# Kernel optimization log

Hardware: AMD Instinct MI355X
Metric: run time of the kernel (lower is better)

Reference implementation:

```python
import jax, jax.numpy as jnp
import numpy as np

T, R, I = 16384, 1024, 128   # time steps, reservoir size, input size
CONN, SR = 0.05, 0.9         # connectivity_rate, spectral_radius


def _make_reservoir(rng):
    # Faithful to ESN.create_reservoir_weights: uniform[0,1), sparsify by
    # connectivity_rate, rescale to target spectral radius, flip half the
    # entries' signs.
    W = rng.random((R, R)).astype(np.float32)
    W[rng.random((R, R)) > CONN] = 0.0
    cur_sr = np.max(np.abs(np.linalg.eigvals(W)))
    W = W * (SR / cur_sr)
    neg = rng.choice(R * R, (R * R) // 2, replace=False)
    Wf = W.reshape(-1).copy()
    Wf[neg] *= -1.0
    return Wf.reshape(R, R).astype(np.float32)


def setup_inputs() -> dict:
    rng = np.random.default_rng(0)
    W_res = jnp.asarray(_make_reservoir(rng))
    key = jax.random.key(0)
    k1, k2 = jax.random.split(key)
    X = jax.random.normal(k1, (T, I), dtype=jnp.float32)
    # nn.init.uniform_(w, a=-1, b=1)
    W_in = jax.random.uniform(k2, (R, I), dtype=jnp.float32, minval=-1.0, maxval=1.0)
    state0 = jnp.zeros((R,), dtype=jnp.float32)
    return {"X": X, "W_in": W_in, "W_res": W_res, "state0": state0}


def reference(X, W_in, W_res, state0):
    # state_t = tanh(W_in @ x_t + W_res @ state_{t-1}); collect all states (T, R).
    # Input projections are independent across time -> one big GEMM up front.
    U = X @ W_in.T  # (T, R)

    def step(s, u):
        s = jnp.tanh(u + W_res @ s)
        return s, s

    _, all_states = jax.lax.scan(step, state0, U)
    return all_states  # (T, R), matches update_state's all_states
```

## Files before the change

kernel.cpp:

```cpp
#include <hip/hip_runtime.h>
#include <hip/hip_bf16.h>
#include <stdint.h>


constexpr int T_N = 16384;
constexpr int R_N = 1024;
constexpr int I_N = 128;

constexpr int BT = 64, BR = 64;

__global__ __launch_bounds__(256) void gemm_u_kernel(
    const float* __restrict__ X, const float* __restrict__ Win,
    float* __restrict__ U)
{
    __shared__ float XS[BT][68];
    __shared__ float WS[BR][68];
    const int tid = threadIdx.x;
    const int ty = tid >> 4, tx = tid & 15;
    const int t0 = blockIdx.x * BT;
    const int r0 = blockIdx.y * BR;
    float acc[4][4] = {};

    for (int k0 = 0; k0 < I_N; k0 += 64) {
        for (int idx = tid; idx < BT * 16; idx += 256) {
            int row = idx >> 4, c4 = (idx & 15) << 2;
            *reinterpret_cast<float4*>(&XS[row][c4]) =
                *reinterpret_cast<const float4*>(&X[(size_t)(t0 + row) * I_N + k0 + c4]);
        }
        for (int idx = tid; idx < BR * 16; idx += 256) {
            int row = idx >> 4, c4 = (idx & 15) << 2;
            *reinterpret_cast<float4*>(&WS[row][c4]) =
                *reinterpret_cast<const float4*>(&Win[(size_t)(r0 + row) * I_N + k0 + c4]);
        }
        __syncthreads();
#pragma unroll
        for (int k = 0; k < 64; k += 4) {
            float4 a[4], b[4];
#pragma unroll
            for (int i = 0; i < 4; ++i)
                a[i] = *reinterpret_cast<const float4*>(&XS[ty + 16 * i][k]);
#pragma unroll
            for (int jj = 0; jj < 4; ++jj)
                b[jj] = *reinterpret_cast<const float4*>(&WS[tx + 16 * jj][k]);
#pragma unroll
            for (int i = 0; i < 4; ++i)
#pragma unroll
                for (int jj = 0; jj < 4; ++jj)
                    acc[i][jj] += a[i].x * b[jj].x + a[i].y * b[jj].y +
                                  a[i].z * b[jj].z + a[i].w * b[jj].w;
        }
        __syncthreads();
    }
#pragma unroll
    for (int i = 0; i < 4; ++i)
#pragma unroll
        for (int jj = 0; jj < 4; ++jj)
            U[(size_t)(t0 + ty + 16 * i) * R_N + (r0 + tx + 16 * jj)] = acc[i][jj];
}

constexpr int GBLK    = 8;
constexpr int NLAUNCH = 64;
constexpr int B2      = 1024;
constexpr int RPB     = R_N / GBLK;
constexpr int TPR     = 8;
constexpr int KMAX    = 96;
constexpr int NSL     = KMAX / TPR;
constexpr int PCAP    = 1 << 20;

__device__ __forceinline__ float fast_tanh(float x) {
    float ax = fabsf(x);
    float e  = __expf(-2.0f * ax);
    float y  = (1.0f - e) / (1.0f + e);
    return copysignf(y, x);
}

__device__ __forceinline__ uint32_t l2_atomic_read(uint32_t* addr) {
    uint32_t old;
    asm volatile("global_atomic_add %0, %1, %2, off sc0\n\t"
                 "s_waitcnt vmcnt(0)"
                 : "=v"(old) : "v"(addr), "v"(0u) : "memory");
    return old;
}

__device__ __forceinline__ void l2_store_u32(uint32_t* addr, uint32_t v) {
    asm volatile("global_store_dword %0, %1, off"
                 :: "v"(addr), "v"(v) : "memory");
}

__global__ __launch_bounds__(1024) void esn_scan_kernel(
    const float* __restrict__ Wres, const float* __restrict__ state0,
    float* out, uint32_t* hdr, uint32_t* slots)
{
    __shared__ int   s_role;
    __shared__ float sbufA[2][R_N];
    __shared__ float sbufB[2][R_N];
    __shared__ uint2 ell[RPB][KMAX];
    __shared__ int   cnt[RPB];
    __shared__ int   rowmap[RPB];
    __shared__ int   hist[KMAX + 1];

    const int tid = threadIdx.x;

    if (tid == 0) {
        uint32_t xcd;
        asm volatile("s_getreg_b32 %0, hwreg(HW_REG_XCC_ID)" : "=s"(xcd));
        xcd &= 7u;
        uint32_t rank = __hip_atomic_fetch_add(&hdr[xcd], 1u,
                            __ATOMIC_RELAXED, __HIP_MEMORY_SCOPE_AGENT);
        int role = -1;
        if (rank < (uint32_t)GBLK) {
            if (rank == (uint32_t)(GBLK - 1)) {
                uint32_t expected = 0u;
                __hip_atomic_compare_exchange_strong(&hdr[8], &expected, xcd + 1u,
                    __ATOMIC_RELAXED, __ATOMIC_RELAXED, __HIP_MEMORY_SCOPE_AGENT);
            }
            uint32_t win = 0; int sp = 0;
            do {
                win = __hip_atomic_load(&hdr[8], __ATOMIC_RELAXED,
                                        __HIP_MEMORY_SCOPE_AGENT);
            } while (win == 0u && ++sp < PCAP);
            if (win == xcd + 1u) role = (int)rank;
        }
        s_role = role;
    }
    __syncthreads();
    const int b = s_role;
    if (b < 0) return;
    const int row0 = b * RPB;

    if (tid < RPB) cnt[tid] = 0;
    __syncthreads();
    for (int idx = tid; idx < RPB * R_N; idx += B2) {
        int r = idx >> 10, c = idx & (R_N - 1);
        float w = Wres[(size_t)(row0 + r) * R_N + c];
        if (w != 0.0f) {
            int slot = atomicAdd(&cnt[r], 1);
            if (slot < KMAX) ell[r][slot] = make_uint2((uint32_t)c, __float_as_uint(w));
        }
    }
    __syncthreads();

    if (tid <= KMAX) hist[tid] = 0;
    __syncthreads();
    if (tid < RPB) atomicAdd(&hist[min(cnt[tid], KMAX)], 1);
    __syncthreads();
    if (tid == 0) {
        int run = 0;
        for (int i = 0; i <= KMAX; ++i) { int c = hist[i]; hist[i] = run; run += c; }
    }
    __syncthreads();
    if (tid < RPB) {
        int c = min(cnt[tid], KMAX);
        int pos = atomicAdd(&hist[c], 1);
        rowmap[pos] = tid;
    }
    __syncthreads();

    const int rloc = rowmap[tid >> 3];
    const int j    = tid & 7;
    const int row  = row0 + rloc;
    const bool oddlane = (tid & 1) != 0;
    int   cols[NSL];
    float vals[NSL];
    int   kw;
    {
        int myn = cnt[rloc];
        if (myn > KMAX) myn = KMAX;
        int kcnt = (myn > j) ? (((myn - 1 - j) >> 3) + 1) : 0;
#pragma unroll
        for (int k = 0; k < NSL; ++k) {
            int slot = j + k * TPR;
            if (slot < myn) {
                uint2 e = ell[rloc][slot];
                int c = (int)e.x;
                if (oddlane) c = (c + 1) & (R_N - 1);
                cols[k] = c;
                vals[k] = __uint_as_float(e.y);
            } else { cols[k] = 0; vals[k] = 0.0f; }
        }
        kw = kcnt;
#pragma unroll
        for (int off = 1; off < 64; off <<= 1) {
            int o = __shfl_xor(kw, off, 64);
            kw = (o > kw) ? o : kw;
        }
        kw = __builtin_amdgcn_readfirstlane(kw);
    }

    sbufA[1][tid] = state0[tid];
    sbufB[1][(tid + 1) & (R_N - 1)] = state0[tid];
    float u_cur = (j == 0) ? out[row] : 0.0f;
    __syncthreads();

    for (int t = 0; t < T_N; ++t) {
        const int p = (t - 1) & 1;

        float u_next = 0.0f;
        if (j == 0 && t + 1 < T_N) u_next = out[(size_t)(t + 1) * R_N + row];

        if (t > 0 && (tid >> 7) != b) {
            uint32_t* slot = slots + ((size_t)p << 10) + tid;
            const uint32_t want8 = (uint32_t)(t & 0xFF);
            uint32_t w; int sp = 0;
            do { w = l2_atomic_read(slot);
            } while ((w & 0xFFu) != want8 && ++sp < PCAP);
            float v = __uint_as_float(w & 0xFFFFFF00u);
            sbufA[p][tid] = v;
            sbufB[p][(tid + 1) & (R_N - 1)] = v;
        }
        __syncthreads();

        const float* sb = oddlane ? sbufB[p] : sbufA[p];
        float acc = 0.0f;
#pragma unroll
        for (int k = 0; k < NSL; ++k) {
            if (k >= kw) break;
            acc = fmaf(vals[k], sb[cols[k]], acc);
        }

        acc += __shfl_xor(acc, 1, TPR);
        acc += __shfl_xor(acc, 2, TPR);
        acc += __shfl_xor(acc, 4, TPR);

        if (j == 0) {
            float y = fast_tanh(u_cur + acc);
            uint32_t bits = __float_as_uint(y);
            uint32_t pkt  = ((bits + 0x80u) & 0xFFFFFF00u)
                          | ((uint32_t)(t + 1) & 0xFFu);
            l2_store_u32(slots + ((size_t)(t & 1) << 10) + row, pkt);
            out[(size_t)t * R_N + row] = y;
            sbufA[t & 1][row] = y;
            sbufB[t & 1][(row + 1) & (R_N - 1)] = y;
        }
        u_cur = u_next;
    }
}

extern "C" void kernel_launch(void* const* d_in, const int* in_sizes, int n_in,
                              void* d_out, int out_size, void* d_ws, size_t ws_size,
                              hipStream_t stream)
{
    const float* X      = (const float*)d_in[0];
    const float* W_in   = (const float*)d_in[1];
    const float* W_res  = (const float*)d_in[2];
    const float* state0 = (const float*)d_in[3];
    float* out = (float*)d_out;

    uint32_t* hdr   = (uint32_t*)d_ws;
    uint32_t* slots = (uint32_t*)((char*)d_ws + 1024);

    hipMemsetAsync(d_ws, 0, 1024 + (size_t)2 * R_N * sizeof(uint32_t), stream);

    dim3 g1(T_N / BT, R_N / BR);
    gemm_u_kernel<<<g1, 256, 0, stream>>>(X, W_in, out);

    esn_scan_kernel<<<NLAUNCH, B2, 0, stream>>>(W_res, state0, out, hdr, slots);
}
```

Baseline: 26.23 ms.

## Prefetch next-step remote state slots early and sort ELL columns by LDS bank

Right after the barrier, each remote thread now issues a non-blocking atomic read of the next step's slot, so the L2 round trip overlaps with the sparse matvec and tanh. A blocking poll runs only if the prefetched value carries a stale tag. The duplicated shifted shared-memory buffer for odd lanes is dropped. Instead, each thread's ELL entries are sorted by bank offset relative to the thread id to cut LDS bank conflicts. The risk is that the early speculative read often sees stale data and still needs the polling loop, and the sorting network adds register pressure.

```diff
diff --git a/kernel.cpp b/kernel.cpp
--- a/kernel.cpp
+++ b/kernel.cpp
@@ -82,6 +82,11 @@
     return old;
 }
 
+__device__ __forceinline__ void l2_atomic_read_issue(uint32_t* addr, uint32_t& dst) {
+    asm volatile("global_atomic_add %0, %1, %2, off sc0"
+                 : "=v"(dst) : "v"(addr), "v"(0u) : "memory");
+}
+
 __device__ __forceinline__ void l2_store_u32(uint32_t* addr, uint32_t v) {
     asm volatile("global_store_dword %0, %1, off"
                  :: "v"(addr), "v"(v) : "memory");
@@ -92,8 +97,7 @@
     float* out, uint32_t* hdr, uint32_t* slots)
 {
     __shared__ int   s_role;
-    __shared__ float sbufA[2][R_N];
-    __shared__ float sbufB[2][R_N];
+    __shared__ float sbuf[2][R_N];
     __shared__ uint2 ell[RPB][KMAX];
     __shared__ int   cnt[RPB];
     __shared__ int   rowmap[RPB];
@@ -159,7 +163,6 @@
     const int rloc = rowmap[tid >> 3];
     const int j    = tid & 7;
     const int row  = row0 + rloc;
-    const bool oddlane = (tid & 1) != 0;
     int   cols[NSL];
     float vals[NSL];
     int   kw;
@@ -167,17 +170,30 @@
         int myn = cnt[rloc];
         if (myn > KMAX) myn = KMAX;
         int kcnt = (myn > j) ? (((myn - 1 - j) >> 3) + 1) : 0;
+        int key[NSL];
 #pragma unroll
         for (int k = 0; k < NSL; ++k) {
             int slot = j + k * TPR;
             if (slot < myn) {
                 uint2 e = ell[rloc][slot];
-                int c = (int)e.x;
-                if (oddlane) c = (c + 1) & (R_N - 1);
-                cols[k] = c;
+                cols[k] = (int)e.x;
                 vals[k] = __uint_as_float(e.y);
-            } else { cols[k] = 0; vals[k] = 0.0f; }
-        }
+                key[k]  = (cols[k] - tid) & 31;
+            } else {
+                cols[k] = tid & (R_N - 1);
+                vals[k] = 0.0f;
+                key[k]  = 32 + k;
+            }
+        }
+#pragma unroll
+        for (int a = 0; a < NSL - 1; ++a)
+#pragma unroll
+            for (int c2 = a + 1; c2 < NSL; ++c2) {
+                bool sw = key[c2] < key[a];
+                int   tk = key[a];  key[a]  = sw ? key[c2]  : key[a];  key[c2]  = sw ? tk : key[c2];
+                int   tc = cols[a]; cols[a] = sw ? cols[c2] : cols[a]; cols[c2] = sw ? tc : cols[c2];
+                float tv = vals[a]; vals[a] = sw ? vals[c2] : vals[a]; vals[c2] = sw ? tv : vals[c2];
+            }
         kw = kcnt;
 #pragma unroll
         for (int off = 1; off < 64; off <<= 1) {
@@ -187,30 +203,41 @@
         kw = __builtin_amdgcn_readfirstlane(kw);
     }
 
-    sbufA[1][tid] = state0[tid];
-    sbufB[1][(tid + 1) & (R_N - 1)] = state0[tid];
+    sbuf[1][tid] = state0[tid];
     float u_cur = (j == 0) ? out[row] : 0.0f;
     __syncthreads();
+
+    const bool remote = (tid >> 7) != b;
+    uint32_t w_pre = 0;
 
     for (int t = 0; t < T_N; ++t) {
         const int p = (t - 1) & 1;
 
+        if (t > 0 && remote) {
+            asm volatile("s_waitcnt vmcnt(0)" : "+v"(w_pre) :: "memory");
+            __builtin_amdgcn_sched_barrier(0);
+            const uint32_t want8 = (uint32_t)(t & 0xFF);
+            uint32_t w = w_pre;
+            if ((w & 0xFFu) != want8) {
+                uint32_t* slot = slots + ((size_t)p << 10) + tid;
+                int sp = 0;
+                do { w = l2_atomic_read(slot);
+                } while ((w & 0xFFu) != want8 && ++sp < PCAP);
+            }
+            sbuf[p][tid] = __uint_as_float(w & 0xFFFFFF00u);
+        }
+
         float u_next = 0.0f;
-        if (j == 0 && t + 1 < T_N) u_next = out[(size_t)(t + 1) * R_N + row];
-
-        if (t > 0 && (tid >> 7) != b) {
-            uint32_t* slot = slots + ((size_t)p << 10) + tid;
-            const uint32_t want8 = (uint32_t)(t & 0xFF);
-            uint32_t w; int sp = 0;
-            do { w = l2_atomic_read(slot);
-            } while ((w & 0xFFu) != want8 && ++sp < PCAP);
-            float v = __uint_as_float(w & 0xFFFFFF00u);
-            sbufA[p][tid] = v;
-            sbufB[p][(tid + 1) & (R_N - 1)] = v;
-        }
+        if (j == 0 && t + 1 < T_N)
+            u_next = out[(size_t)(t + 1) * R_N + row];
+
         __syncthreads();
 
-        const float* sb = oddlane ? sbufB[p] : sbufA[p];
+        if (remote && t + 1 < T_N)
+            l2_atomic_read_issue(
+                slots + ((size_t)(t & 1) << 10) + tid, w_pre);
+
+        const float* sb = sbuf[p];
         float acc = 0.0f;
 #pragma unroll
         for (int k = 0; k < NSL; ++k) {
@@ -229,8 +256,7 @@
                           | ((uint32_t)(t + 1) & 0xFFu);
             l2_store_u32(slots + ((size_t)(t & 1) << 10) + row, pkt);
             out[(size_t)t * R_N + row] = y;
-            sbufA[t & 1][row] = y;
-            sbufB[t & 1][(row + 1) & (R_N - 1)] = y;
+            sbuf[t & 1][row] = y;
         }
         u_cur = u_next;
     }
```

Measured after the change: 26.32 ms. No clear change (+0.4%).

## Poll two state slots per 64-bit atomic and drop row sorting and bank-shift buffers

Applied to the files above, without the earlier changes.

The cross-block polling now reads two adjacent packed state values with one 64-bit L2 atomic, so only half the threads poll and each does half as many atomic round trips per step. The duplicated shifted shared buffer (sbufB), the odd-lane column offset, and the row sorting by nonzero count are removed, leaving a single state buffer and a per-thread loop bound. This trades the wave-uniform loop bound and bank-conflict avoidance for fewer polling atomics and simpler LDS writes, which may add divergence or bank conflicts in the sparse gather.

```diff
diff --git a/kernel.cpp b/kernel.cpp
--- a/kernel.cpp
+++ b/kernel.cpp
@@ -65,6 +65,7 @@
 constexpr int TPR     = 8;
 constexpr int KMAX    = 96;
 constexpr int NSL     = KMAX / TPR;
+constexpr int NSLOT   = R_N / 2;
 constexpr int PCAP    = 1 << 20;
 
 __device__ __forceinline__ float fast_tanh(float x) {
@@ -74,11 +75,13 @@
     return copysignf(y, x);
 }
 
-__device__ __forceinline__ uint32_t l2_atomic_read(uint32_t* addr) {
-    uint32_t old;
-    asm volatile("global_atomic_add %0, %1, %2, off sc0\n\t"
+__device__ __forceinline__ unsigned long long l2_atomic_read64(
+    unsigned long long* addr)
+{
+    unsigned long long old;
+    asm volatile("global_atomic_add_x2 %0, %1, %2, off sc0\n\t"
                  "s_waitcnt vmcnt(0)"
-                 : "=v"(old) : "v"(addr), "v"(0u) : "memory");
+                 : "=v"(old) : "v"(addr), "v"(0ull) : "memory");
     return old;
 }
 
@@ -89,15 +92,12 @@
 
 __global__ __launch_bounds__(1024) void esn_scan_kernel(
     const float* __restrict__ Wres, const float* __restrict__ state0,
-    float* out, uint32_t* hdr, uint32_t* slots)
+    float* out, uint32_t* hdr, unsigned long long* slots)
 {
     __shared__ int   s_role;
-    __shared__ float sbufA[2][R_N];
-    __shared__ float sbufB[2][R_N];
+    __shared__ float sbuf[2][R_N];
     __shared__ uint2 ell[RPB][KMAX];
     __shared__ int   cnt[RPB];
-    __shared__ int   rowmap[RPB];
-    __shared__ int   hist[KMAX + 1];
 
     const int tid = threadIdx.x;
 
@@ -140,57 +140,33 @@
     }
     __syncthreads();
 
-    if (tid <= KMAX) hist[tid] = 0;
-    __syncthreads();
-    if (tid < RPB) atomicAdd(&hist[min(cnt[tid], KMAX)], 1);
-    __syncthreads();
-    if (tid == 0) {
-        int run = 0;
-        for (int i = 0; i <= KMAX; ++i) { int c = hist[i]; hist[i] = run; run += c; }
-    }
-    __syncthreads();
-    if (tid < RPB) {
-        int c = min(cnt[tid], KMAX);
-        int pos = atomicAdd(&hist[c], 1);
-        rowmap[pos] = tid;
-    }
-    __syncthreads();
-
-    const int rloc = rowmap[tid >> 3];
+    const int rloc = tid >> 3;
     const int j    = tid & 7;
     const int row  = row0 + rloc;
-    const bool oddlane = (tid & 1) != 0;
     int   cols[NSL];
     float vals[NSL];
-    int   kw;
+    int   kcnt;
     {
         int myn = cnt[rloc];
         if (myn > KMAX) myn = KMAX;
-        int kcnt = (myn > j) ? (((myn - 1 - j) >> 3) + 1) : 0;
+        kcnt = (myn > j) ? (((myn - 1 - j) >> 3) + 1) : 0;
 #pragma unroll
         for (int k = 0; k < NSL; ++k) {
             int slot = j + k * TPR;
             if (slot < myn) {
                 uint2 e = ell[rloc][slot];
-                int c = (int)e.x;
-                if (oddlane) c = (c + 1) & (R_N - 1);
-                cols[k] = c;
+                cols[k] = (int)e.x;
                 vals[k] = __uint_as_float(e.y);
             } else { cols[k] = 0; vals[k] = 0.0f; }
         }
-        kw = kcnt;
-#pragma unroll
-        for (int off = 1; off < 64; off <<= 1) {
-            int o = __shfl_xor(kw, off, 64);
-            kw = (o > kw) ? o : kw;
-        }
-        kw = __builtin_amdgcn_readfirstlane(kw);
-    }
-
-    sbufA[1][tid] = state0[tid];
-    sbufB[1][(tid + 1) & (R_N - 1)] = state0[tid];
+    }
+
+    sbuf[1][tid] = state0[tid];
     float u_cur = (j == 0) ? out[row] : 0.0f;
     __syncthreads();
+
+    const bool poller = (tid < NSLOT) && ((tid >> 6) != b);
+    uint32_t* const slots4 = (uint32_t*)slots;
 
     for (int t = 0; t < T_N; ++t) {
         const int p = (t - 1) & 1;
@@ -198,25 +174,27 @@
         float u_next = 0.0f;
         if (j == 0 && t + 1 < T_N) u_next = out[(size_t)(t + 1) * R_N + row];
 
-        if (t > 0 && (tid >> 7) != b) {
-            uint32_t* slot = slots + ((size_t)p << 10) + tid;
+        if (t > 0 && poller) {
+            unsigned long long* slot = slots + ((size_t)p << 9) + tid;
             const uint32_t want8 = (uint32_t)(t & 0xFF);
-            uint32_t w; int sp = 0;
-            do { w = l2_atomic_read(slot);
-            } while ((w & 0xFFu) != want8 && ++sp < PCAP);
-            float v = __uint_as_float(w & 0xFFFFFF00u);
-            sbufA[p][tid] = v;
-            sbufB[p][(tid + 1) & (R_N - 1)] = v;
+            const unsigned long long want2 =
+                (unsigned long long)want8 | ((unsigned long long)want8 << 32);
+            const unsigned long long tmask = 0x000000FF000000FFull;
+            unsigned long long w; int sp = 0;
+            do { w = l2_atomic_read64(slot);
+            } while (((w ^ want2) & tmask) != 0ull && ++sp < PCAP);
+            float2 st;
+            st.x = __uint_as_float((uint32_t)w & 0xFFFFFF00u);
+            st.y = __uint_as_float((uint32_t)(w >> 32) & 0xFFFFFF00u);
+            *reinterpret_cast<float2*>(&sbuf[p][tid << 1]) = st;
         }
         __syncthreads();
 
-        const float* sb = oddlane ? sbufB[p] : sbufA[p];
+        const float* sb = sbuf[p];
         float acc = 0.0f;
 #pragma unroll
-        for (int k = 0; k < NSL; ++k) {
-            if (k >= kw) break;
-            acc = fmaf(vals[k], sb[cols[k]], acc);
-        }
+        for (int k = 0; k < NSL; ++k)
+            if (k < kcnt) acc = fmaf(vals[k], sb[cols[k]], acc);
 
         acc += __shfl_xor(acc, 1, TPR);
         acc += __shfl_xor(acc, 2, TPR);
@@ -227,10 +205,9 @@
             uint32_t bits = __float_as_uint(y);
             uint32_t pkt  = ((bits + 0x80u) & 0xFFFFFF00u)
                           | ((uint32_t)(t + 1) & 0xFFu);
-            l2_store_u32(slots + ((size_t)(t & 1) << 10) + row, pkt);
+            l2_store_u32(slots4 + ((size_t)(t & 1) << 10) + row, pkt);
             out[(size_t)t * R_N + row] = y;
-            sbufA[t & 1][row] = y;
-            sbufB[t & 1][(row + 1) & (R_N - 1)] = y;
+            sbuf[t & 1][row] = y;
         }
         u_cur = u_next;
     }
@@ -246,10 +223,12 @@
     const float* state0 = (const float*)d_in[3];
     float* out = (float*)d_out;
 
-    uint32_t* hdr   = (uint32_t*)d_ws;
-    uint32_t* slots = (uint32_t*)((char*)d_ws + 1024);
-
-    hipMemsetAsync(d_ws, 0, 1024 + (size_t)2 * R_N * sizeof(uint32_t), stream);
+    uint32_t* hdr = (uint32_t*)d_ws;
+    unsigned long long* slots =
+        (unsigned long long*)((char*)d_ws + 1024);
+
+    hipMemsetAsync(d_ws, 0, 1024 + (size_t)2 * NSLOT * sizeof(unsigned long long),
+                   stream);
 
     dim3 g1(T_N / BT, R_N / BR);
     gemm_u_kernel<<<g1, 256, 0, stream>>>(X, W_in, out);
```

Result: faster. 24.15 ms (-7.9%).
